# Kernel optimization log

Measured on AMD Instinct MI355X. Metric: run time of the kernel, lower is better.

## Reference

```python
import jax, jax.numpy as jnp
import numpy as np

D_MODEL = 256
N_HEADS = 8
N_LEVELS = 4
N_POINTS = 4
HEAD_DIM = D_MODEL // N_HEADS
SPATIAL = [(64, 64), (32, 32), (16, 16), (8, 8)]
LEN_IN = sum(h * w for h, w in SPATIAL)
BATCH = 4
LEN_Q = LEN_IN


def _offset_bias():
    # replicate the module's _reset_parameters grid init for sampling_offsets.bias
    th = np.arange(N_HEADS, dtype=np.float64) * (2.0 * np.pi / N_HEADS)
    g = np.stack([np.cos(th), np.sin(th)], -1)
    g = g / np.abs(g).max(-1, keepdims=True)
    g = np.tile(g[:, None, None, :], (1, N_LEVELS, N_POINTS, 1))
    g = g * (np.arange(N_POINTS) + 1)[None, None, :, None]
    return jnp.asarray(g.reshape(-1), jnp.float32)


def setup_inputs() -> dict:
    key = jax.random.key(0)
    ks = jax.random.split(key, 10)
    s = 1.0 / np.sqrt(D_MODEL)
    return {
        "query": jax.random.normal(ks[0], (BATCH, LEN_Q, D_MODEL), jnp.float32),
        "reference_points": jax.random.uniform(ks[1], (BATCH, LEN_Q, N_LEVELS, 2), jnp.float32),
        "input_flatten": jax.random.normal(ks[2], (BATCH, LEN_IN, D_MODEL), jnp.float32),
        "input_spatial_shapes": np.array(SPATIAL, dtype=np.int64),
        "input_level_start_index": np.cumsum([0] + [h * w for h, w in SPATIAL[:-1]]).astype(np.int64),
        "W_val": jax.random.normal(ks[3], (D_MODEL, D_MODEL), jnp.float32) * s,
        "b_val": jnp.zeros((D_MODEL,), jnp.float32),
        "W_off": jax.random.normal(ks[4], (D_MODEL, N_HEADS * N_LEVELS * N_POINTS * 2), jnp.float32) * 0.01,
        "b_off": _offset_bias(),
        "W_attn": jax.random.normal(ks[5], (D_MODEL, N_HEADS * N_LEVELS * N_POINTS), jnp.float32) * 0.01,
        "b_attn": jnp.zeros((N_HEADS * N_LEVELS * N_POINTS,), jnp.float32),
        "W_out": jax.random.normal(ks[6], (D_MODEL, D_MODEL), jnp.float32) * s,
        "b_out": jnp.zeros((D_MODEL,), jnp.float32),
    }


def bilinear_sample(v, grid):
    # v: [B, C, H, W]; grid: [B, Q, P, 2] normalized to [-1, 1] (x=W axis, y=H axis)
    # matches torch F.grid_sample(mode='bilinear', padding_mode='zeros', align_corners=False)
    B, C, H, W = v.shape
    x = (grid[..., 0] + 1.0) * (W * 0.5) - 0.5
    y = (grid[..., 1] + 1.0) * (H * 0.5) - 0.5
    x0 = jnp.floor(x)
    y0 = jnp.floor(y)
    wx = x - x0
    wy = y - y0
    v_flat = v.reshape(B, C, H * W)

    def corner(xi, yi, wgt):
        valid = (xi >= 0) & (xi <= W - 1) & (yi >= 0) & (yi <= H - 1)
        xc = jnp.clip(xi, 0, W - 1).astype(jnp.int32)
        yc = jnp.clip(yi, 0, H - 1).astype(jnp.int32)
        idx = (yc * W + xc).reshape(B, 1, -1)
        g = jnp.take_along_axis(v_flat, jnp.broadcast_to(idx, (B, C, idx.shape[-1])), axis=2)
        return g * (wgt * valid).reshape(B, 1, -1)

    out = (corner(x0, y0, (1 - wx) * (1 - wy))
           + corner(x0 + 1, y0, wx * (1 - wy))
           + corner(x0, y0 + 1, (1 - wx) * wy)
           + corner(x0 + 1, y0 + 1, wx * wy))
    return out.reshape(B, C, grid.shape[1], grid.shape[2])


def reference(query, reference_points, input_flatten, input_spatial_shapes,
              input_level_start_index, W_val, b_val, W_off, b_off,
              W_attn, b_attn, W_out, b_out):
    ss = np.asarray(input_spatial_shapes)  # static [L, 2] (H, W)
    Nb, Lq, _ = query.shape
    value = (input_flatten @ W_val + b_val).reshape(Nb, -1, N_HEADS, HEAD_DIM)
    off = (query @ W_off + b_off).reshape(Nb, Lq, N_HEADS, N_LEVELS, N_POINTS, 2)
    attn = (query @ W_attn + b_attn).reshape(Nb, Lq, N_HEADS, N_LEVELS * N_POINTS)
    attn = jax.nn.softmax(attn, -1).reshape(Nb, Lq, N_HEADS, N_LEVELS, N_POINTS)
    # offset normalizer: (W, H) per level
    normalizer = jnp.asarray(ss[:, ::-1].copy(), jnp.float32)
    loc = reference_points[:, :, None, :, None, :] + off / normalizer[None, None, None, :, None, :]
    grids = 2.0 * loc - 1.0  # [N, Lq, H, L, P, 2]
    splits = np.cumsum([int(h) * int(w) for h, w in ss])[:-1]
    value_list = jnp.split(value, splits, axis=1)
    out = jnp.zeros((Nb * N_HEADS, HEAD_DIM, Lq), query.dtype)
    for lid, (h, w) in enumerate(ss):
        h, w = int(h), int(w)
        v = value_list[lid].transpose(0, 2, 3, 1).reshape(Nb * N_HEADS, HEAD_DIM, h, w)
        g = grids[:, :, :, lid].transpose(0, 2, 1, 3, 4).reshape(Nb * N_HEADS, Lq, N_POINTS, 2)
        sampled = bilinear_sample(v, g)  # [N*H, D, Lq, P]
        aw = attn[:, :, :, lid].transpose(0, 2, 1, 3).reshape(Nb * N_HEADS, 1, Lq, N_POINTS)
        out = out + (sampled * aw).sum(-1)
    out = out.reshape(Nb, N_HEADS * HEAD_DIM, Lq).transpose(0, 2, 1)
    return out @ W_out + b_out
```

## Files before the change

kernel.cpp:

```cpp
#include <hip/hip_runtime.h>
#include <hip/hip_bf16.h>
#include <math.h>

typedef unsigned short ushort_t;
typedef __attribute__((ext_vector_type(8))) short bf16x8;
typedef __attribute__((ext_vector_type(4))) float f32x4;
typedef __attribute__((ext_vector_type(2))) float f32x2;

constexpr int BATCH   = 4;
constexpr int D_MODEL = 256;
constexpr int LEN_IN  = 5440;
constexpr int LEN_Q   = 5440;
constexpr int M_TOT   = BATCH * LEN_Q;

#define ASG __attribute__((address_space(1)))
#define ASL __attribute__((address_space(3)))

__device__ __forceinline__ void gld16(const void* g, void* l) {
    __builtin_amdgcn_global_load_lds((ASG const void*)g, (ASL void*)l, 16, 0, 0);
}

__device__ __forceinline__ ushort_t bfbits(float x) {
    __hip_bfloat16 h = __float2bfloat16(x);
    ushort_t u; __builtin_memcpy(&u, &h, 2); return u;
}
__device__ __forceinline__ unsigned pk2(float a, float b) {
    return (unsigned)bfbits(a) | ((unsigned)bfbits(b) << 16);
}

__global__ __launch_bounds__(256) void pack_inputs(
    const float* __restrict__ inflat, const float* __restrict__ query,
    const float* __restrict__ Wv, const float* __restrict__ Wo,
    const float* __restrict__ Wa, const float* __restrict__ Wout,
    const float* __restrict__ b_off, const float* __restrict__ b_attn,
    ushort_t* __restrict__ in_bf, ushort_t* __restrict__ q_bf,
    ushort_t* __restrict__ wvT, ushort_t* __restrict__ woaT,
    ushort_t* __restrict__ woutT, float* __restrict__ bias_oa)
{
    const int blk = blockIdx.x, tid = threadIdx.x;
    if (blk < 5440) {
        const float* src = (blk < 2720) ? inflat : query;
        ushort_t*    dst = (blk < 2720) ? in_bf : q_bf;
        const int rb = (blk < 2720) ? blk : blk - 2720;
        const size_t base = (size_t)rb * 2048 + tid * 8;
        float4 a = *(const float4*)(src + base);
        float4 b = *(const float4*)(src + base + 4);
        uint4 o;
        o.x = pk2(a.x, a.y); o.y = pk2(a.z, a.w);
        o.z = pk2(b.x, b.y); o.w = pk2(b.z, b.w);
        *(uint4*)(dst + base) = o;
    } else if (blk < 5504) {
        const float* src = (blk < 5472) ? Wv : Wout;
        ushort_t*    dst = (blk < 5472) ? wvT : woutT;
        const int base = (blk - ((blk < 5472) ? 5440 : 5472)) * 2048;
#pragma unroll
        for (int i = 0; i < 8; i++) {
            const int idx = base + i * 256 + tid;
            const int k = idx >> 8, n = idx & 255;
            dst[n * 256 + k] = bfbits(src[idx]);
        }
    } else if (blk < 5552) {
        const int base = (blk - 5504) * 2048;
#pragma unroll
        for (int i = 0; i < 8; i++) {
            const int idx = base + i * 256 + tid;
            const int k = idx / 384, j = idx - k * 384;
            const float v = (j < 256) ? Wo[k * 256 + j] : Wa[k * 128 + (j - 256)];
            woaT[j * 256 + k] = bfbits(v);
        }
    } else {
        bias_oa[tid] = b_off[tid];
        if (tid < 128) bias_oa[256 + tid] = b_attn[tid];
    }
}

template <int OUT_MODE>
__device__ __forceinline__ void gemm_core(
    const ushort_t* __restrict__ A, const ushort_t* __restrict__ BT,
    const float* __restrict__ bias, void* __restrict__ Cp, int N,
    int bm, int bn, ushort_t* As, ushort_t* Bs)
{
    const int tid  = threadIdx.x;
    const int wave = tid >> 6, lane = tid & 63;
    const int wm = (wave >> 1) * 64, wn = (wave & 1) * 64;
    const int c0 = 2 * wave, c1 = 2 * wave + 1;
    const int kb = (lane & 3) * 8;
    const ushort_t* gA0 = A  + (size_t)(bm + c0 * 16 + (lane >> 2)) * 256 + kb;
    const ushort_t* gA1 = A  + (size_t)(bm + c1 * 16 + (lane >> 2)) * 256 + kb;
    const ushort_t* gB0 = BT + (size_t)(bn + c0 * 16 + (lane >> 2)) * 256 + kb;
    const ushort_t* gB1 = BT + (size_t)(bn + c1 * 16 + (lane >> 2)) * 256 + kb;
    ushort_t* lA0 = As + c0 * 512;
    ushort_t* lA1 = As + c1 * 512;
    ushort_t* lB0 = Bs + c0 * 512;
    ushort_t* lB1 = Bs + c1 * 512;

    f32x4 acc[4][4] = {};

    const int row = lane & 15, kg = (lane >> 4) * 8;
    for (int kt = 0; kt < 8; kt++) {
        gld16(gA0, lA0); gld16(gA1, lA1);
        gld16(gB0, lB0); gld16(gB1, lB1);
        gA0 += 32; gA1 += 32; gB0 += 32; gB1 += 32;
        __syncthreads();
        bf16x8 af[4], bfr[4];
#pragma unroll
        for (int i = 0; i < 4; i++)
            af[i] = *(const bf16x8*)(As + (wm + i * 16 + row) * 32 + kg);
#pragma unroll
        for (int j = 0; j < 4; j++)
            bfr[j] = *(const bf16x8*)(Bs + (wn + j * 16 + row) * 32 + kg);
#pragma unroll
        for (int i = 0; i < 4; i++)
#pragma unroll
            for (int j = 0; j < 4; j++)
                acc[i][j] = __builtin_amdgcn_mfma_f32_16x16x32_bf16(
                    af[i], bfr[j], acc[i][j], 0, 0, 0);
        __syncthreads();
    }

    const int col = lane & 15, rbase = (lane >> 4) * 4;
#pragma unroll
    for (int j = 0; j < 4; j++) {
        const int cc = bn + wn + j * 16 + col;
        const float bv = bias[cc];
#pragma unroll
        for (int i = 0; i < 4; i++) {
            const int rr = bm + wm + i * 16 + rbase;
#pragma unroll
            for (int r = 0; r < 4; r++) {
                const float v = acc[i][j][r] + bv;
                const int m = rr + r;
                if (OUT_MODE == 0) {
                    ((float*)Cp)[(size_t)m * N + cc] = v;
                } else if (OUT_MODE == 1) {
                    ((ushort_t*)Cp)[(size_t)m * N + cc] = bfbits(v);
                } else {
                    const int bb  = m / LEN_IN;
                    const int pix = m - bb * LEN_IN;
                    const int head = cc >> 5, ch = cc & 31;
                    ((ushort_t*)Cp)[((size_t)((bb * 8 + head) * LEN_IN + pix) << 5) + ch] = bfbits(v);
                }
            }
        }
    }
}

__global__ __launch_bounds__(256) void gemm_dual(
    const ushort_t* __restrict__ in_bf, const ushort_t* __restrict__ wvT,
    const float* __restrict__ b_val, ushort_t* __restrict__ value_bf,
    const ushort_t* __restrict__ q_bf, const ushort_t* __restrict__ woaT,
    const float* __restrict__ bias_oa, float* __restrict__ offattn)
{
    __shared__ ushort_t As[128 * 32];
    __shared__ ushort_t Bs[128 * 32];
    int blk = blockIdx.x;
    if (blk < 340) {
        const int bn = (blk & 1) * 128, bm = (blk >> 1) * 128;
        gemm_core<2>(in_bf, wvT, b_val, value_bf, 256, bm, bn, As, Bs);
    } else {
        blk -= 340;
        const int bn = (blk % 3) * 128, bm = (blk / 3) * 128;
        gemm_core<0>(q_bf, woaT, bias_oa, offattn, 384, bm, bn, As, Bs);
    }
}

__global__ __launch_bounds__(256) void gemm_out(
    const ushort_t* __restrict__ mid_bf, const ushort_t* __restrict__ woutT,
    const float* __restrict__ b_out, float* __restrict__ out)
{
    __shared__ ushort_t As[128 * 32];
    __shared__ ushort_t Bs[128 * 32];
    const int bn = (blockIdx.x & 1) * 128, bm = (blockIdx.x >> 1) * 128;
    gemm_core<0>(mid_bf, woutT, b_out, out, 256, bm, bn, As, Bs);
}

__device__ __forceinline__ void accd(f32x2& a, unsigned u, f32x2 w) {
    f32x2 v;
    v.x = __uint_as_float(u << 16);
    v.y = __uint_as_float(u & 0xFFFF0000u);
    a = w * v + a;
}
__device__ __forceinline__ void acc_corner(f32x2* a, uint4 A, uint4 B, uint4 C, uint4 D, float wf) {
    const f32x2 w = {wf, wf};
    accd(a[0],  A.x, w); accd(a[1],  A.y, w); accd(a[2],  A.z, w); accd(a[3],  A.w, w);
    accd(a[4],  B.x, w); accd(a[5],  B.y, w); accd(a[6],  B.z, w); accd(a[7],  B.w, w);
    accd(a[8],  C.x, w); accd(a[9],  C.y, w); accd(a[10], C.z, w); accd(a[11], C.w, w);
    accd(a[12], D.x, w); accd(a[13], D.y, w); accd(a[14], D.z, w); accd(a[15], D.w, w);
}

__global__ __launch_bounds__(256) void msda_sample_v2(
    const ushort_t* __restrict__ value,
    const float* __restrict__ refp,
    const float* __restrict__ offattn,
    ushort_t* __restrict__ mid)
{
    __shared__ float4 part[8][256];

    const int tid = threadIdx.x;
    const unsigned bid = blockIdx.x;
    const int xcd   = bid & 7;
    const int pos   = bid >> 3;
    const int slice = pos / 85;
    const int qc    = pos - slice * 85;
    const int bh    = xcd * 4 + slice;
    const int b     = bh >> 3, h = bh & 7;

    const int ql = tid >> 2;
    const int pl = tid & 3;
    const int q  = qc * 64 + ql;
    const int bq = b * LEN_Q + q;

    const int   shift = 6 - pl;
    const int   W     = 1 << shift;
    const float fW    = (float)W;
    const float invW  = __uint_as_float((unsigned)(127 - shift) << 23);
    const int   st    = (pl == 0) ? 0 : (pl == 1) ? 4096 : (pl == 2) ? 5120 : 5376;

    const float2 rr2 = *(const float2*)(refp + (size_t)bq * 8 + pl * 2);
    const float* oab = offattn + (size_t)bq * 384;
    const float4 o01 = *(const float4*)(oab + h * 32 + pl * 8);
    const float4 o23 = *(const float4*)(oab + h * 32 + pl * 8 + 4);
    const float4 lg  = *(const float4*)(oab + 256 + h * 16 + pl * 4);

    float mx = fmaxf(fmaxf(lg.x, lg.y), fmaxf(lg.z, lg.w));
    mx = fmaxf(mx, __shfl_xor(mx, 1));
    mx = fmaxf(mx, __shfl_xor(mx, 2));

    const char* vbc = (const char*)(value + (size_t)bh * (LEN_IN * 32));

    f32x2 acc2[16];
#pragma unroll
    for (int d = 0; d < 16; d++) acc2[d] = (f32x2){0.f, 0.f};
    float esum = 0.f;

    const float oxA[4] = {o01.x, o01.z, o23.x, o23.z};
    const float oyA[4] = {o01.y, o01.w, o23.y, o23.w};
    const float lgA[4] = {lg.x, lg.y, lg.z, lg.w};

#pragma unroll
    for (int p = 0; p < 4; p++) {
        const float x = (rr2.x + oxA[p] * invW) * fW - 0.5f;
        const float y = (rr2.y + oyA[p] * invW) * fW - 0.5f;
        const float x0f = floorf(x), y0f = floorf(y);
        const float wx = x - x0f, wy = y - y0f;
        const int ix0 = (int)x0f, iy0 = (int)y0f;
        const int ix1 = ix0 + 1,  iy1 = iy0 + 1;
        const float vx0 = (ix0 >= 0 && ix0 < W) ? 1.f : 0.f;
        const float vx1 = (ix1 >= 0 && ix1 < W) ? 1.f : 0.f;
        const float vy0 = (iy0 >= 0 && iy0 < W) ? 1.f : 0.f;
        const float vy1 = (iy1 >= 0 && iy1 < W) ? 1.f : 0.f;
        const int cx0 = min(max(ix0, 0), W - 1);
        const int cx1 = min(max(ix1, 0), W - 1);
        const int cy0 = min(max(iy0, 0), W - 1);
        const int cy1 = min(max(iy1, 0), W - 1);
        const float hx0 = (1.f - wx) * vx0, hx1 = wx * vx1;
        const float hy0 = (1.f - wy) * vy0, hy1 = wy * vy1;

        const float e = __expf(lgA[p] - mx);
        esum += e;
        const float w00 = e * hx0 * hy0, w01 = e * hx1 * hy0;
        const float w10 = e * hx0 * hy1, w11 = e * hx1 * hy1;

        const int r0 = st + (cy0 << shift), r1 = st + (cy1 << shift);
        const uint4* c00 = (const uint4*)(vbc + ((size_t)(r0 + cx0) << 6));
        const uint4* c01 = (const uint4*)(vbc + ((size_t)(r0 + cx1) << 6));
        const uint4* c10 = (const uint4*)(vbc + ((size_t)(r1 + cx0) << 6));
        const uint4* c11 = (const uint4*)(vbc + ((size_t)(r1 + cx1) << 6));
        uint4 A0 = c00[0], A1 = c00[1], A2 = c00[2], A3 = c00[3];
        uint4 B0 = c01[0], B1 = c01[1], B2 = c01[2], B3 = c01[3];
        uint4 C0 = c10[0], C1 = c10[1], C2 = c10[2], C3 = c10[3];
        uint4 D0 = c11[0], D1 = c11[1], D2 = c11[2], D3 = c11[3];

        acc_corner(acc2, A0, A1, A2, A3, w00);
        acc_corner(acc2, B0, B1, B2, B3, w01);
        acc_corner(acc2, C0, C1, C2, C3, w10);
        acc_corner(acc2, D0, D1, D2, D3, w11);
    }

    esum += __shfl_xor(esum, 1);
    esum += __shfl_xor(esum, 2);

#pragma unroll
    for (int j = 0; j < 8; j++)
        part[j][tid] = make_float4(acc2[2 * j].x, acc2[2 * j].y,
                                   acc2[2 * j + 1].x, acc2[2 * j + 1].y);

    const int j0 = pl * 2;
    const int lb = tid & ~3;
    float4 s0 = part[j0][lb], s1 = part[j0 + 1][lb];
#pragma unroll
    for (int pp = 1; pp < 4; pp++) {
        const float4 t0 = part[j0][lb + pp];
        const float4 t1 = part[j0 + 1][lb + pp];
        s0.x += t0.x; s0.y += t0.y; s0.z += t0.z; s0.w += t0.w;
        s1.x += t1.x; s1.y += t1.y; s1.z += t1.z; s1.w += t1.w;
    }

    const float inv = 1.f / esum;
    uint4 o;
    o.x = pk2(s0.x * inv, s0.y * inv);
    o.y = pk2(s0.z * inv, s0.w * inv);
    o.z = pk2(s1.x * inv, s1.y * inv);
    o.w = pk2(s1.z * inv, s1.w * inv);
    *(uint4*)(mid + (size_t)bq * 256 + h * 32 + pl * 8) = o;
}

extern "C" void kernel_launch(void* const* d_in, const int* in_sizes, int n_in,
                              void* d_out, int out_size, void* d_ws, size_t ws_size,
                              hipStream_t stream)
{
    const float* query  = (const float*)d_in[0];
    const float* refp   = (const float*)d_in[1];
    const float* inflat = (const float*)d_in[2];
    const float* W_val  = (const float*)d_in[5];
    const float* b_val  = (const float*)d_in[6];
    const float* W_off  = (const float*)d_in[7];
    const float* W_attn = (const float*)d_in[9];
    const float* b_off  = (const float*)d_in[8];
    const float* b_attn = (const float*)d_in[10];
    const float* W_out  = (const float*)d_in[11];
    const float* b_out  = (const float*)d_in[12];
    float* out = (float*)d_out;

    char* ws = (char*)d_ws;
    ushort_t* in_bf    = (ushort_t*)ws;
    ushort_t* q_bf     = (ushort_t*)(ws + 11141120);
    ushort_t* value_bf = (ushort_t*)(ws + 22282240);
    ushort_t* wvT      = (ushort_t*)(ws + 33423360);
    ushort_t* woutT    = (ushort_t*)(ws + 33554432);
    ushort_t* woaT     = (ushort_t*)(ws + 33685504);
    float*    bias_oa  = (float*)   (ws + 33882112);
    float*    offattn  = (float*)   (ws + 33883648);
    ushort_t* mid_bf   = in_bf;

    dim3 blk(256);
    pack_inputs<<<dim3(5553), blk, 0, stream>>>(
        inflat, query, W_val, W_off, W_attn, W_out, b_off, b_attn,
        in_bf, q_bf, wvT, woaT, woutT, bias_oa);
    gemm_dual<<<dim3(850), blk, 0, stream>>>(
        in_bf, wvT, b_val, value_bf, q_bf, woaT, bias_oa, offattn);
    msda_sample_v2<<<dim3(2720), blk, 0, stream>>>(
        value_bf, refp, offattn, mid_bf);
    gemm_out<<<dim3(340), blk, 0, stream>>>(
        mid_bf, woutT, b_out, out);
}
```

Baseline: 215.5 us.

## Split sampling work by channel group instead of level, dropping LDS reduction

The sampling kernel now gives each of the four lanes per query an 8-channel slice across all 4 levels and 16 points, instead of one level with all 32 channels. This removes the shared-memory partial-sum reduction and cuts per-thread accumulator registers from 32 to 8. In exchange, each lane recomputes the bilinear coordinates, softmax and offsets for all 16 samples, so coordinate math and offset/logit loads are duplicated fourfold. Each corner fetch becomes one 16-byte load per lane, and the four lanes of a query read adjacent 16-byte pieces of the same 64-byte row.

```diff
diff --git a/kernel.cpp b/kernel.cpp
--- a/kernel.cpp
+++ b/kernel.cpp
@@ -180,22 +180,18 @@
     v.y = __uint_as_float(u & 0xFFFF0000u);
     a = w * v + a;
 }
-__device__ __forceinline__ void acc_corner(f32x2* a, uint4 A, uint4 B, uint4 C, uint4 D, float wf) {
+__device__ __forceinline__ void accp(f32x2* a, uint4 u, float wf) {
     const f32x2 w = {wf, wf};
-    accd(a[0],  A.x, w); accd(a[1],  A.y, w); accd(a[2],  A.z, w); accd(a[3],  A.w, w);
-    accd(a[4],  B.x, w); accd(a[5],  B.y, w); accd(a[6],  B.z, w); accd(a[7],  B.w, w);
-    accd(a[8],  C.x, w); accd(a[9],  C.y, w); accd(a[10], C.z, w); accd(a[11], C.w, w);
-    accd(a[12], D.x, w); accd(a[13], D.y, w); accd(a[14], D.z, w); accd(a[15], D.w, w);
-}
-
-__global__ __launch_bounds__(256) void msda_sample_v2(
+    accd(a[0], u.x, w); accd(a[1], u.y, w);
+    accd(a[2], u.z, w); accd(a[3], u.w, w);
+}
+
+__global__ __launch_bounds__(256) void msda_sample_v3(
     const ushort_t* __restrict__ value,
     const float* __restrict__ refp,
     const float* __restrict__ offattn,
     ushort_t* __restrict__ mid)
 {
-    __shared__ float4 part[8][256];
-
     const int tid = threadIdx.x;
     const unsigned bid = blockIdx.x;
     const int xcd   = bid & 7;
@@ -206,103 +202,93 @@
     const int b     = bh >> 3, h = bh & 7;
 
     const int ql = tid >> 2;
-    const int pl = tid & 3;
-    const int q  = qc * 64 + ql;
-    const int bq = b * LEN_Q + q;
-
-    const int   shift = 6 - pl;
-    const int   W     = 1 << shift;
-    const float fW    = (float)W;
-    const float invW  = __uint_as_float((unsigned)(127 - shift) << 23);
-    const int   st    = (pl == 0) ? 0 : (pl == 1) ? 4096 : (pl == 2) ? 5120 : 5376;
-
-    const float2 rr2 = *(const float2*)(refp + (size_t)bq * 8 + pl * 2);
+    const int cg = tid & 3;
+    const int bq = b * LEN_Q + qc * 64 + ql;
+
     const float* oab = offattn + (size_t)bq * 384;
-    const float4 o01 = *(const float4*)(oab + h * 32 + pl * 8);
-    const float4 o23 = *(const float4*)(oab + h * 32 + pl * 8 + 4);
-    const float4 lg  = *(const float4*)(oab + 256 + h * 16 + pl * 4);
-
-    float mx = fmaxf(fmaxf(lg.x, lg.y), fmaxf(lg.z, lg.w));
-    mx = fmaxf(mx, __shfl_xor(mx, 1));
-    mx = fmaxf(mx, __shfl_xor(mx, 2));
-
-    const char* vbc = (const char*)(value + (size_t)bh * (LEN_IN * 32));
-
-    f32x2 acc2[16];
-#pragma unroll
-    for (int d = 0; d < 16; d++) acc2[d] = (f32x2){0.f, 0.f};
+    const float* lp = oab + 256 + h * 16;
+    float4 l0 = ((const float4*)lp)[0];
+    float4 l1 = ((const float4*)lp)[1];
+    float4 l2 = ((const float4*)lp)[2];
+    float4 l3 = ((const float4*)lp)[3];
+    float lg[16] = {l0.x, l0.y, l0.z, l0.w, l1.x, l1.y, l1.z, l1.w,
+                    l2.x, l2.y, l2.z, l2.w, l3.x, l3.y, l3.z, l3.w};
+    float mx = lg[0];
+#pragma unroll
+    for (int j = 1; j < 16; j++) mx = fmaxf(mx, lg[j]);
+
+    const float* op = oab + h * 32;
+    float4 ov[8];
+#pragma unroll
+    for (int j = 0; j < 8; j++) ov[j] = ((const float4*)op)[j];
+    const float* rp = refp + (size_t)bq * 8;
+    float4 r0 = ((const float4*)rp)[0];
+    float4 r1 = ((const float4*)rp)[1];
+    const float rx[4] = {r0.x, r0.z, r1.x, r1.z};
+    const float ry[4] = {r0.y, r0.w, r1.y, r1.w};
+
+    const char* vb = (const char*)value + (size_t)bh * (LEN_IN * 64) + cg * 16;
+
+    f32x2 acc2[4];
+#pragma unroll
+    for (int d = 0; d < 4; d++) acc2[d] = (f32x2){0.f, 0.f};
     float esum = 0.f;
 
-    const float oxA[4] = {o01.x, o01.z, o23.x, o23.z};
-    const float oyA[4] = {o01.y, o01.w, o23.y, o23.w};
-    const float lgA[4] = {lg.x, lg.y, lg.z, lg.w};
-
-#pragma unroll
-    for (int p = 0; p < 4; p++) {
-        const float x = (rr2.x + oxA[p] * invW) * fW - 0.5f;
-        const float y = (rr2.y + oyA[p] * invW) * fW - 0.5f;
-        const float x0f = floorf(x), y0f = floorf(y);
-        const float wx = x - x0f, wy = y - y0f;
-        const int ix0 = (int)x0f, iy0 = (int)y0f;
-        const int ix1 = ix0 + 1,  iy1 = iy0 + 1;
-        const float vx0 = (ix0 >= 0 && ix0 < W) ? 1.f : 0.f;
-        const float vx1 = (ix1 >= 0 && ix1 < W) ? 1.f : 0.f;
-        const float vy0 = (iy0 >= 0 && iy0 < W) ? 1.f : 0.f;
-        const float vy1 = (iy1 >= 0 && iy1 < W) ? 1.f : 0.f;
-        const int cx0 = min(max(ix0, 0), W - 1);
-        const int cx1 = min(max(ix1, 0), W - 1);
-        const int cy0 = min(max(iy0, 0), W - 1);
-        const int cy1 = min(max(iy1, 0), W - 1);
-        const float hx0 = (1.f - wx) * vx0, hx1 = wx * vx1;
-        const float hy0 = (1.f - wy) * vy0, hy1 = wy * vy1;
-
-        const float e = __expf(lgA[p] - mx);
-        esum += e;
-        const float w00 = e * hx0 * hy0, w01 = e * hx1 * hy0;
-        const float w10 = e * hx0 * hy1, w11 = e * hx1 * hy1;
-
-        const int r0 = st + (cy0 << shift), r1 = st + (cy1 << shift);
-        const uint4* c00 = (const uint4*)(vbc + ((size_t)(r0 + cx0) << 6));
-        const uint4* c01 = (const uint4*)(vbc + ((size_t)(r0 + cx1) << 6));
-        const uint4* c10 = (const uint4*)(vbc + ((size_t)(r1 + cx0) << 6));
-        const uint4* c11 = (const uint4*)(vbc + ((size_t)(r1 + cx1) << 6));
-        uint4 A0 = c00[0], A1 = c00[1], A2 = c00[2], A3 = c00[3];
-        uint4 B0 = c01[0], B1 = c01[1], B2 = c01[2], B3 = c01[3];
-        uint4 C0 = c10[0], C1 = c10[1], C2 = c10[2], C3 = c10[3];
-        uint4 D0 = c11[0], D1 = c11[1], D2 = c11[2], D3 = c11[3];
-
-        acc_corner(acc2, A0, A1, A2, A3, w00);
-        acc_corner(acc2, B0, B1, B2, B3, w01);
-        acc_corner(acc2, C0, C1, C2, C3, w10);
-        acc_corner(acc2, D0, D1, D2, D3, w11);
-    }
-
-    esum += __shfl_xor(esum, 1);
-    esum += __shfl_xor(esum, 2);
-
-#pragma unroll
-    for (int j = 0; j < 8; j++)
-        part[j][tid] = make_float4(acc2[2 * j].x, acc2[2 * j].y,
-                                   acc2[2 * j + 1].x, acc2[2 * j + 1].y);
-
-    const int j0 = pl * 2;
-    const int lb = tid & ~3;
-    float4 s0 = part[j0][lb], s1 = part[j0 + 1][lb];
-#pragma unroll
-    for (int pp = 1; pp < 4; pp++) {
-        const float4 t0 = part[j0][lb + pp];
-        const float4 t1 = part[j0 + 1][lb + pp];
-        s0.x += t0.x; s0.y += t0.y; s0.z += t0.z; s0.w += t0.w;
-        s1.x += t1.x; s1.y += t1.y; s1.z += t1.z; s1.w += t1.w;
+#pragma unroll
+    for (int l = 0; l < 4; l++) {
+        const int   shift = 6 - l;
+        const int   W     = 1 << shift;
+        const float fW    = (float)W;
+        const float invW  = __uint_as_float((unsigned)(127 - shift) << 23);
+        const int   st    = (l == 0) ? 0 : (l == 1) ? 4096 : (l == 2) ? 5120 : 5376;
+#pragma unroll
+        for (int p = 0; p < 4; p++) {
+            const float* o2 = &ov[l * 2].x;
+            const float ox = o2[p * 2 + 0];
+            const float oy = o2[p * 2 + 1];
+            const float x = (rx[l] + ox * invW) * fW - 0.5f;
+            const float y = (ry[l] + oy * invW) * fW - 0.5f;
+            const float x0f = floorf(x), y0f = floorf(y);
+            const float wx = x - x0f, wy = y - y0f;
+            const int ix0 = (int)x0f, iy0 = (int)y0f;
+            const int ix1 = ix0 + 1,  iy1 = iy0 + 1;
+            const float vx0 = (ix0 >= 0 && ix0 < W) ? 1.f : 0.f;
+            const float vx1 = (ix1 >= 0 && ix1 < W) ? 1.f : 0.f;
+            const float vy0 = (iy0 >= 0 && iy0 < W) ? 1.f : 0.f;
+            const float vy1 = (iy1 >= 0 && iy1 < W) ? 1.f : 0.f;
+            const int cx0 = min(max(ix0, 0), W - 1);
+            const int cx1 = min(max(ix1, 0), W - 1);
+            const int cy0 = min(max(iy0, 0), W - 1);
+            const int cy1 = min(max(iy1, 0), W - 1);
+            const float hx0 = (1.f - wx) * vx0, hx1 = wx * vx1;
+            const float hy0 = (1.f - wy) * vy0, hy1 = wy * vy1;
+
+            const float e = __expf(lg[l * 4 + p] - mx);
+            esum += e;
+            const float w00 = e * hx0 * hy0, w01 = e * hx1 * hy0;
+            const float w10 = e * hx0 * hy1, w11 = e * hx1 * hy1;
+
+            const int r0a = st + (cy0 << shift);
+            const int r1a = st + (cy1 << shift);
+            uint4 v00 = *(const uint4*)(vb + ((size_t)(r0a + cx0) << 6));
+            uint4 v01 = *(const uint4*)(vb + ((size_t)(r0a + cx1) << 6));
+            uint4 v10 = *(const uint4*)(vb + ((size_t)(r1a + cx0) << 6));
+            uint4 v11 = *(const uint4*)(vb + ((size_t)(r1a + cx1) << 6));
+
+            accp(acc2, v00, w00);
+            accp(acc2, v01, w01);
+            accp(acc2, v10, w10);
+            accp(acc2, v11, w11);
+        }
     }
 
     const float inv = 1.f / esum;
     uint4 o;
-    o.x = pk2(s0.x * inv, s0.y * inv);
-    o.y = pk2(s0.z * inv, s0.w * inv);
-    o.z = pk2(s1.x * inv, s1.y * inv);
-    o.w = pk2(s1.z * inv, s1.w * inv);
-    *(uint4*)(mid + (size_t)bq * 256 + h * 32 + pl * 8) = o;
+    o.x = pk2(acc2[0].x * inv, acc2[0].y * inv);
+    o.y = pk2(acc2[1].x * inv, acc2[1].y * inv);
+    o.z = pk2(acc2[2].x * inv, acc2[2].y * inv);
+    o.w = pk2(acc2[3].x * inv, acc2[3].y * inv);
+    ((uint4*)(mid + (size_t)bq * 256 + h * 32))[cg] = o;
 }
 
 extern "C" void kernel_launch(void* const* d_in, const int* in_sizes, int n_in,
@@ -339,7 +325,7 @@
         in_bf, q_bf, wvT, woaT, woutT, bias_oa);
     gemm_dual<<<dim3(850), blk, 0, stream>>>(
         in_bf, wvT, b_val, value_bf, q_bf, woaT, bias_oa, offattn);
-    msda_sample_v2<<<dim3(2720), blk, 0, stream>>>(
+    msda_sample_v3<<<dim3(2720), blk, 0, stream>>>(
         value_bf, refp, offattn, mid_bf);
     gemm_out<<<dim3(340), blk, 0, stream>>>(
         mid_bf, woutT, b_out, out);
```

After: 195.9 us. 9.1% less time.
